# Optimization experiments

Hardware: AMD Instinct MI355X
Metric: run time of the kernel (lower is better)

Reference implementation:

```python
import jax, jax.numpy as jnp
import numpy as np

G, S, M = 131072, 16, 8  # num_groups, state_dim, measure_dim


def setup_inputs() -> dict:
    key = jax.random.key(0)
    ks = jax.random.split(key, 7)
    inp = jax.random.normal(ks[0], (G, M), jnp.float32)
    mean = jax.random.normal(ks[1], (G, S), jnp.float32)
    a = jax.random.normal(ks[2], (G, S, S), jnp.float32)
    cov = a @ jnp.swapaxes(a, -1, -2) / S + jnp.eye(S, dtype=jnp.float32)  # SPD state cov
    H = jax.random.normal(ks[3], (G, M, S), jnp.float32) * 0.5
    b = jax.random.normal(ks[4], (G, M, M), jnp.float32)
    R = b @ jnp.swapaxes(b, -1, -2) / M + jnp.eye(M, dtype=jnp.float32)  # SPD measure noise
    F = jax.random.normal(ks[5], (G, S, S), jnp.float32) * (0.5 / np.sqrt(S))  # quasi-stable transition
    c = jax.random.normal(ks[6], (G, S, S), jnp.float32)
    Q = c @ jnp.swapaxes(c, -1, -2) / S + 0.1 * jnp.eye(S, dtype=jnp.float32)  # SPD process noise
    return {"input": inp, "mean": mean, "cov": cov, "H": H, "R": R, "F": F, "Q": Q}


def reference(input, mean, cov, H, R, F, Q):
    # --- update (no-NaN path of GaussianStep.update -> _update) ---
    Ht = jnp.swapaxes(H, -1, -2)                     # [G,S,M]
    covHt = cov @ Ht                                 # [G,S,M]
    Ssys = H @ covHt + R                             # innovation covariance [G,M,M]
    # torch: solve(B=covHt^T, A=Ssys^T) then transpose -> K = covHt @ inv(Ssys)
    Kt = jnp.linalg.solve(jnp.swapaxes(Ssys, -1, -2), jnp.swapaxes(covHt, -1, -2))  # [G,M,S]
    K = jnp.swapaxes(Kt, -1, -2)                     # [G,S,M]
    resid = input - jnp.einsum('gms,gs->gm', H, mean)
    new_mean = mean + jnp.einsum('gsm,gm->gs', K, resid)
    I = jnp.eye(S, dtype=cov.dtype)
    ikh = I - K @ H                                  # [G,S,S]
    # stable (Joseph form) covariance update
    new_cov = ikh @ cov @ jnp.swapaxes(ikh, -1, -2) + K @ R @ jnp.swapaxes(K, -1, -2)
    # --- predict ---
    pred_mean = jnp.einsum('gij,gj->gi', F, new_mean)
    pred_cov = F @ new_cov @ jnp.swapaxes(F, -1, -2) + Q
    return pred_mean, pred_cov
```

## Files before the change

### kernel.cpp

```cpp
#include <hip/hip_runtime.h>


typedef float v2f __attribute__((ext_vector_type(2)));
typedef _Float16 h2 __attribute__((ext_vector_type(2)));

__device__ __forceinline__ float bq(float x, int t) {
    switch (t & 3) {
    case 0:  return __int_as_float(__builtin_amdgcn_mov_dpp(__float_as_int(x), 0x00, 0xF, 0xF, true));
    case 1:  return __int_as_float(__builtin_amdgcn_mov_dpp(__float_as_int(x), 0x55, 0xF, 0xF, true));
    case 2:  return __int_as_float(__builtin_amdgcn_mov_dpp(__float_as_int(x), 0xAA, 0xF, 0xF, true));
    default: return __int_as_float(__builtin_amdgcn_mov_dpp(__float_as_int(x), 0xFF, 0xF, 0xF, true));
    }
}
__device__ __forceinline__ v2f splat(float c) { v2f r; r.x = c; r.y = c; return r; }
__device__ __forceinline__ v2f up2(h2 h) { v2f r; r.x = (float)h.x; r.y = (float)h.y; return r; }

__global__ __launch_bounds__(64) void kalman_kernel(
    const float* __restrict__ g_in,
    const float* __restrict__ g_mean,
    const float* __restrict__ g_cov,
    const float* __restrict__ g_H,
    const float* __restrict__ g_R,
    const float* __restrict__ g_F,
    const float* __restrict__ g_Q,
    float* __restrict__ g_out,
    int G)
{
    const int l = threadIdx.x & 3;
    const int g = (blockIdx.x << 4) | (threadIdx.x >> 2);

    const float* const Pp = g_cov + (size_t)g * 256;
    const float* const Hp = g_H   + (size_t)g * 128;
    const float* const Rp = g_R   + (size_t)g * 64;
    const float* const Fp = g_F   + (size_t)g * 256;
    const float* const Qp = g_Q   + (size_t)g * 256;

    v2f Plo[16], Phi[16];
    #pragma unroll
    for (int k = 0; k < 16; ++k) {
        const float4 t = *reinterpret_cast<const float4*>(Pp + k*16 + 4*l);
        Plo[k].x=t.x; Plo[k].y=t.y; Phi[k].x=t.z; Phi[k].y=t.w;
    }
    h2 HT16[16];
    {
        float4 ra[4], rb[4];
        #pragma unroll
        for (int p = 0; p < 4; ++p) {
            ra[p] = *reinterpret_cast<const float4*>(Hp + (2*l  )*16 + 4*p);
            rb[p] = *reinterpret_cast<const float4*>(Hp + (2*l+1)*16 + 4*p);
        }
        #pragma unroll
        for (int p = 0; p < 4; ++p) {
            HT16[4*p+0].x=(_Float16)ra[p].x; HT16[4*p+0].y=(_Float16)rb[p].x;
            HT16[4*p+1].x=(_Float16)ra[p].y; HT16[4*p+1].y=(_Float16)rb[p].y;
            HT16[4*p+2].x=(_Float16)ra[p].z; HT16[4*p+2].y=(_Float16)rb[p].z;
            HT16[4*p+3].x=(_Float16)ra[p].w; HT16[4*p+3].y=(_Float16)rb[p].w;
        }
    }
    v2f resd;
    {
        const float2 it = *reinterpret_cast<const float2*>(g_in + (size_t)g*8 + 2*l);
        const float4 mt = *reinterpret_cast<const float4*>(g_mean + (size_t)g*16 + 4*l);
        resd.x = it.x; resd.y = it.y;
        #pragma unroll
        for (int k = 0; k < 16; ++k) {
            const float m = bq((k&2) ? ((k&1)?mt.w:mt.z) : ((k&1)?mt.y:mt.x), k>>2);
            resd -= splat(m) * up2(HT16[k]);
        }
    }

    v2f CTlo[8], CThi[8];
    #pragma unroll
    for (int i = 0; i < 8; ++i) {
        v2f alo = {0.f,0.f}, ahi = {0.f,0.f};
        #pragma unroll
        for (int k = 0; k < 16; ++k) {
            const float h = bq((float)((i&1) ? HT16[k].y : HT16[k].x), i>>1);
            alo += splat(h) * Plo[k];
            ahi += splat(h) * Phi[k];
        }
        CTlo[i]=alo; CThi[i]=ahi;
    }

    v2f S[8];
    #pragma unroll
    for (int i = 0; i < 8; ++i) {
        const float2 rt = *reinterpret_cast<const float2*>(Rp + i*8 + 2*l);
        v2f acc; acc.x = rt.x; acc.y = rt.y;
        #pragma unroll
        for (int k = 0; k < 16; ++k) {
            const float c = bq((k&2) ? ((k&1)?CThi[i].y:CThi[i].x)
                                     : ((k&1)?CTlo[i].y:CTlo[i].x), k>>2);
            acc += splat(c) * up2(HT16[k]);
        }
        S[i] = acc;
    }

    #pragma unroll
    for (int k = 0; k < 8; ++k) {
        const float p    = bq((k&1) ? S[k].y : S[k].x, k>>1);
        const float pinv = __builtin_amdgcn_rcpf(p);
        S[k] *= splat(pinv);
        S[k].x = (2*l   == k) ? pinv : S[k].x;
        S[k].y = (2*l+1 == k) ? pinv : S[k].y;
        #pragma unroll
        for (int i = 0; i < 8; ++i) {
            if (i == k) continue;
            const float f  = bq((k&1) ? S[i].y : S[i].x, k>>1);
            const float nf = -f * pinv;
            S[i] -= splat(f) * S[k];
            S[i].x = (2*l   == k) ? nf : S[i].x;
            S[i].y = (2*l+1 == k) ? nf : S[i].y;
        }
    }

    v2f nmL, nmH;
    {
        const float4 mt = *reinterpret_cast<const float4*>(g_mean + (size_t)g*16 + 4*l);
        nmL.x=mt.x; nmL.y=mt.y; nmH.x=mt.z; nmH.y=mt.w;
    }
    #pragma unroll
    for (int m = 0; m < 8; ++m) {
        v2f xlo = {0.f,0.f}, xhi = {0.f,0.f};
        #pragma unroll
        for (int j = 0; j < 8; ++j) {
            const float s = bq((j&1) ? S[m].y : S[m].x, j>>1);
            xlo += splat(s) * CTlo[j];
            xhi += splat(s) * CThi[j];
        }
        const float r = bq((m&1) ? resd.y : resd.x, m>>1);
        nmL += splat(r) * xlo;
        nmH += splat(r) * xhi;
        #pragma unroll
        for (int s2 = 0; s2 < 16; ++s2) {
            const float c = bq((s2&2) ? ((s2&1)?CThi[m].y:CThi[m].x)
                                      : ((s2&1)?CTlo[m].y:CTlo[m].x), s2>>2);
            Plo[s2] -= splat(c) * xlo;
            Phi[s2] -= splat(c) * xhi;
        }
    }
    __builtin_amdgcn_sched_barrier(0);

    h2 FT16a[16], FT16b[16];
    {
        #pragma unroll
        for (int p = 0; p < 4; ++p) {
            const float4 r0 = *reinterpret_cast<const float4*>(Fp + (4*l+0)*16 + 4*p);
            const float4 r1 = *reinterpret_cast<const float4*>(Fp + (4*l+1)*16 + 4*p);
            const float4 r2 = *reinterpret_cast<const float4*>(Fp + (4*l+2)*16 + 4*p);
            const float4 r3 = *reinterpret_cast<const float4*>(Fp + (4*l+3)*16 + 4*p);
            FT16a[4*p+0].x=(_Float16)r0.x; FT16a[4*p+0].y=(_Float16)r1.x;
            FT16b[4*p+0].x=(_Float16)r2.x; FT16b[4*p+0].y=(_Float16)r3.x;
            FT16a[4*p+1].x=(_Float16)r0.y; FT16a[4*p+1].y=(_Float16)r1.y;
            FT16b[4*p+1].x=(_Float16)r2.y; FT16b[4*p+1].y=(_Float16)r3.y;
            FT16a[4*p+2].x=(_Float16)r0.z; FT16a[4*p+2].y=(_Float16)r1.z;
            FT16b[4*p+2].x=(_Float16)r2.z; FT16b[4*p+2].y=(_Float16)r3.z;
            FT16a[4*p+3].x=(_Float16)r0.w; FT16a[4*p+3].y=(_Float16)r1.w;
            FT16b[4*p+3].x=(_Float16)r2.w; FT16b[4*p+3].y=(_Float16)r3.w;
        }
    }

    {
        v2f plo = {0.f,0.f}, phi = {0.f,0.f};
        #pragma unroll
        for (int k = 0; k < 16; ++k) {
            const float m = bq((k&2) ? ((k&1)?nmH.y:nmH.x)
                                     : ((k&1)?nmL.y:nmL.x), k>>2);
            plo += splat(m) * up2(FT16a[k]);
            phi += splat(m) * up2(FT16b[k]);
        }
        *reinterpret_cast<float4*>(g_out + (size_t)g*16 + 4*l) =
            make_float4(plo.x, plo.y, phi.x, phi.y);
    }

    float* const out_pc = g_out + (size_t)G*16 + (size_t)g*256;
    float4 qbuf[2];
    #pragma unroll
    for (int i = 0; i < 2; ++i)
        qbuf[i] = *reinterpret_cast<const float4*>(Qp + i*16 + 4*l);
    #pragma unroll
    for (int i = 0; i < 16; ++i) {
        v2f wlo = {0.f,0.f}, whi = {0.f,0.f};
        #pragma unroll
        for (int k = 0; k < 16; ++k) {
            const float f = bq((float)((i&2) ? ((i&1)?FT16b[k].y:FT16b[k].x)
                                             : ((i&1)?FT16a[k].y:FT16a[k].x)), i>>2);
            wlo += splat(f) * Plo[k];
            whi += splat(f) * Phi[k];
        }
        const float4 qv = qbuf[i & 1];
        if (i + 2 < 16)
            qbuf[i & 1] = *reinterpret_cast<const float4*>(Qp + (i+2)*16 + 4*l);
        v2f olo; olo.x=qv.x; olo.y=qv.y;
        v2f ohi; ohi.x=qv.z; ohi.y=qv.w;
        #pragma unroll
        for (int t = 0; t < 16; ++t) {
            const float wb = bq((t&2) ? ((t&1)?whi.y:whi.x)
                                      : ((t&1)?wlo.y:wlo.x), t>>2);
            olo += splat(wb) * up2(FT16a[t]);
            ohi += splat(wb) * up2(FT16b[t]);
        }
        *reinterpret_cast<float4*>(out_pc + i*16 + 4*l) =
            make_float4(olo.x, olo.y, ohi.x, ohi.y);
    }
}

extern "C" void kernel_launch(void* const* d_in, const int* in_sizes, int n_in,
                              void* d_out, int out_size, void* d_ws, size_t ws_size,
                              hipStream_t stream) {
    const float* g_in   = (const float*)d_in[0];
    const float* g_mean = (const float*)d_in[1];
    const float* g_cov  = (const float*)d_in[2];
    const float* g_H    = (const float*)d_in[3];
    const float* g_R    = (const float*)d_in[4];
    const float* g_F    = (const float*)d_in[5];
    const float* g_Q    = (const float*)d_in[6];
    float* out = (float*)d_out;
    const int G = in_sizes[2] / 256;
    kalman_kernel<<<G/16, 64, 0, stream>>>(g_in, g_mean, g_cov, g_H, g_R, g_F, g_Q, out, G);
}
```

Before: 147.2 us.

## Stream cov into CT accumulation, park cov as fp16, keep H in fp32, use 256-thread blocks

The state covariance is no longer held in fp32 registers for the whole solve. It is streamed in row by row while computing cov·Hᵀ and kept packed as fp16 until the Joseph-style update, where it is expanded back to fp32. H is now kept in fp32 instead of fp16, the Q prefetch depth grows from 2 to 4 rows, and blocks grow from 64 to 256 threads covering 64 groups. The goal is lower peak register pressure for better occupancy and more latency hiding. The cost is extra fp16 rounding of the prior covariance, which adds numerical error.

```diff
diff --git a/kernel.cpp b/kernel.cpp
--- a/kernel.cpp
+++ b/kernel.cpp
@@ -14,8 +14,9 @@
 }
 __device__ __forceinline__ v2f splat(float c) { v2f r; r.x = c; r.y = c; return r; }
 __device__ __forceinline__ v2f up2(h2 h) { v2f r; r.x = (float)h.x; r.y = (float)h.y; return r; }
-
-__global__ __launch_bounds__(64) void kalman_kernel(
+__device__ __forceinline__ h2 pk2(v2f v) { h2 r; r.x = (_Float16)v.x; r.y = (_Float16)v.y; return r; }
+
+__global__ __launch_bounds__(256) void kalman_kernel(
     const float* __restrict__ g_in,
     const float* __restrict__ g_mean,
     const float* __restrict__ g_cov,
@@ -27,7 +28,7 @@
     int G)
 {
     const int l = threadIdx.x & 3;
-    const int g = (blockIdx.x << 4) | (threadIdx.x >> 2);
+    const int g = (blockIdx.x << 6) | (threadIdx.x >> 2);
 
     const float* const Pp = g_cov + (size_t)g * 256;
     const float* const Hp = g_H   + (size_t)g * 128;
@@ -35,13 +36,7 @@
     const float* const Fp = g_F   + (size_t)g * 256;
     const float* const Qp = g_Q   + (size_t)g * 256;
 
-    v2f Plo[16], Phi[16];
-    #pragma unroll
-    for (int k = 0; k < 16; ++k) {
-        const float4 t = *reinterpret_cast<const float4*>(Pp + k*16 + 4*l);
-        Plo[k].x=t.x; Plo[k].y=t.y; Phi[k].x=t.z; Phi[k].y=t.w;
-    }
-    h2 HT16[16];
+    v2f HT[16];
     {
         float4 ra[4], rb[4];
         #pragma unroll
@@ -51,10 +46,10 @@
         }
         #pragma unroll
         for (int p = 0; p < 4; ++p) {
-            HT16[4*p+0].x=(_Float16)ra[p].x; HT16[4*p+0].y=(_Float16)rb[p].x;
-            HT16[4*p+1].x=(_Float16)ra[p].y; HT16[4*p+1].y=(_Float16)rb[p].y;
-            HT16[4*p+2].x=(_Float16)ra[p].z; HT16[4*p+2].y=(_Float16)rb[p].z;
-            HT16[4*p+3].x=(_Float16)ra[p].w; HT16[4*p+3].y=(_Float16)rb[p].w;
+            HT[4*p+0].x=ra[p].x; HT[4*p+0].y=rb[p].x;
+            HT[4*p+1].x=ra[p].y; HT[4*p+1].y=rb[p].y;
+            HT[4*p+2].x=ra[p].z; HT[4*p+2].y=rb[p].z;
+            HT[4*p+3].x=ra[p].w; HT[4*p+3].y=rb[p].w;
         }
     }
     v2f resd;
@@ -65,21 +60,34 @@
         #pragma unroll
         for (int k = 0; k < 16; ++k) {
             const float m = bq((k&2) ? ((k&1)?mt.w:mt.z) : ((k&1)?mt.y:mt.x), k>>2);
-            resd -= splat(m) * up2(HT16[k]);
+            resd -= splat(m) * HT[k];
         }
     }
 
     v2f CTlo[8], CThi[8];
     #pragma unroll
-    for (int i = 0; i < 8; ++i) {
-        v2f alo = {0.f,0.f}, ahi = {0.f,0.f};
-        #pragma unroll
-        for (int k = 0; k < 16; ++k) {
-            const float h = bq((float)((i&1) ? HT16[k].y : HT16[k].x), i>>1);
-            alo += splat(h) * Plo[k];
-            ahi += splat(h) * Phi[k];
-        }
-        CTlo[i]=alo; CThi[i]=ahi;
+    for (int i = 0; i < 8; ++i) { CTlo[i] = splat(0.f); CThi[i] = splat(0.f); }
+    h2 PF16a[16], PF16b[16];
+    #pragma unroll
+    for (int p = 0; p < 4; ++p) {
+        float4 c[4];
+        #pragma unroll
+        for (int r = 0; r < 4; ++r)
+            c[r] = *reinterpret_cast<const float4*>(Pp + (4*p+r)*16 + 4*l);
+        #pragma unroll
+        for (int r = 0; r < 4; ++r) {
+            const int k = 4*p + r;
+            v2f plo, phi;
+            plo.x=c[r].x; plo.y=c[r].y; phi.x=c[r].z; phi.y=c[r].w;
+            #pragma unroll
+            for (int i = 0; i < 8; ++i) {
+                const float h = bq((i&1) ? HT[k].y : HT[k].x, i>>1);
+                CTlo[i] += splat(h) * plo;
+                CThi[i] += splat(h) * phi;
+            }
+            PF16a[k] = pk2(plo);
+            PF16b[k] = pk2(phi);
+        }
     }
 
     v2f S[8];
@@ -91,7 +99,7 @@
         for (int k = 0; k < 16; ++k) {
             const float c = bq((k&2) ? ((k&1)?CThi[i].y:CThi[i].x)
                                      : ((k&1)?CTlo[i].y:CTlo[i].x), k>>2);
-            acc += splat(c) * up2(HT16[k]);
+            acc += splat(c) * HT[k];
         }
         S[i] = acc;
     }
@@ -114,6 +122,12 @@
         }
     }
 
+    v2f NClo[16], NChi[16];
+    #pragma unroll
+    for (int k = 0; k < 16; ++k) {
+        NClo[k] = up2(PF16a[k]);
+        NChi[k] = up2(PF16b[k]);
+    }
     v2f nmL, nmH;
     {
         const float4 mt = *reinterpret_cast<const float4*>(g_mean + (size_t)g*16 + 4*l);
@@ -135,8 +149,8 @@
         for (int s2 = 0; s2 < 16; ++s2) {
             const float c = bq((s2&2) ? ((s2&1)?CThi[m].y:CThi[m].x)
                                       : ((s2&1)?CTlo[m].y:CTlo[m].x), s2>>2);
-            Plo[s2] -= splat(c) * xlo;
-            Phi[s2] -= splat(c) * xhi;
+            NClo[s2] -= splat(c) * xlo;
+            NChi[s2] -= splat(c) * xhi;
         }
     }
     __builtin_amdgcn_sched_barrier(0);
@@ -174,9 +188,9 @@
     }
 
     float* const out_pc = g_out + (size_t)G*16 + (size_t)g*256;
-    float4 qbuf[2];
-    #pragma unroll
-    for (int i = 0; i < 2; ++i)
+    float4 qbuf[4];
+    #pragma unroll
+    for (int i = 0; i < 4; ++i)
         qbuf[i] = *reinterpret_cast<const float4*>(Qp + i*16 + 4*l);
     #pragma unroll
     for (int i = 0; i < 16; ++i) {
@@ -185,12 +199,12 @@
         for (int k = 0; k < 16; ++k) {
             const float f = bq((float)((i&2) ? ((i&1)?FT16b[k].y:FT16b[k].x)
                                              : ((i&1)?FT16a[k].y:FT16a[k].x)), i>>2);
-            wlo += splat(f) * Plo[k];
-            whi += splat(f) * Phi[k];
-        }
-        const float4 qv = qbuf[i & 1];
-        if (i + 2 < 16)
-            qbuf[i & 1] = *reinterpret_cast<const float4*>(Qp + (i+2)*16 + 4*l);
+            wlo += splat(f) * NClo[k];
+            whi += splat(f) * NChi[k];
+        }
+        const float4 qv = qbuf[i & 3];
+        if (i + 4 < 16)
+            qbuf[i & 3] = *reinterpret_cast<const float4*>(Qp + (i+4)*16 + 4*l);
         v2f olo; olo.x=qv.x; olo.y=qv.y;
         v2f ohi; ohi.x=qv.z; ohi.y=qv.w;
         #pragma unroll
@@ -217,5 +231,5 @@
     const float* g_Q    = (const float*)d_in[6];
     float* out = (float*)d_out;
     const int G = in_sizes[2] / 256;
-    kalman_kernel<<<G/16, 64, 0, stream>>>(g_in, g_mean, g_cov, g_H, g_R, g_F, g_Q, out, G);
+    kalman_kernel<<<G/64, 256, 0, stream>>>(g_in, g_mean, g_cov, g_H, g_R, g_F, g_Q, out, G);
 }
```

Result: no change. 144.6 us (-1.7%).
